# Kernel tuning notes

Measured on AMD Instinct MI355X. Metric: run time of the kernel, lower is better.

## Reference

```python
import jax, jax.numpy as jnp
import numpy as np

B_, T, N, C = 1024, 8, 49, 96
NUM_HEADS = 3
NW = 64  # number of distinct window masks


def setup_inputs() -> dict:
    key = jax.random.key(0)
    ks = jax.random.split(key, 8)
    x = jax.random.normal(ks[0], (B_, T, N, C), dtype=jnp.float32)
    # Swin-style additive mask: mostly 0, some large-negative entries
    mask = jnp.where(jax.random.uniform(ks[1], (NW, N, N)) < 0.9, 0.0, -100.0).astype(jnp.float32)
    s = 0.02
    qkv_w = jax.random.normal(ks[2], (C, 3 * C), dtype=jnp.float32) * s
    qkv_b = jnp.zeros((3 * C,), dtype=jnp.float32)
    proj_sp_w = jax.random.normal(ks[3], (C, C), dtype=jnp.float32) * s
    proj_sp_b = jnp.zeros((C,), dtype=jnp.float32)
    proj_temp_w = jax.random.normal(ks[4], (C, C), dtype=jnp.float32) * s
    proj_temp_b = jnp.zeros((C,), dtype=jnp.float32)
    return {
        "x": x, "mask": mask,
        "qkv_w": qkv_w, "qkv_b": qkv_b,
        "proj_sp_w": proj_sp_w, "proj_sp_b": proj_sp_b,
        "proj_temp_w": proj_temp_w, "proj_temp_b": proj_temp_b,
    }


def _attend(xseq, qkv_w, qkv_b, num_heads, scale, mask=None):
    """xseq: (B, L, C). Returns (B, L, C). mask: (nW, L, L) or None."""
    Bt, L, Cd = xseq.shape
    hd = Cd // num_heads
    qkv = (xseq @ qkv_w + qkv_b).reshape(Bt, L, 3, num_heads, hd)
    q, k, v = qkv[:, :, 0], qkv[:, :, 1], qkv[:, :, 2]  # (B, L, H, hd)
    attn = jnp.einsum("bnhd,bmhd->bhnm", q * scale, k)  # (B, H, L, L)
    if mask is not None:
        nW = mask.shape[0]
        attn = attn.reshape(Bt // nW, nW, num_heads, L, L) + mask[None, :, None]
        attn = attn.reshape(Bt, num_heads, L, L)
    attn = jax.nn.softmax(attn, axis=-1)
    out = jnp.einsum("bhnm,bmhd->bnhd", attn, v).reshape(Bt, L, Cd)
    return out


def reference(x, mask, qkv_w, qkv_b, proj_sp_w, proj_sp_b, proj_temp_w, proj_temp_b):
    Bw, Tt, Nn, Cc = x.shape
    hd = Cc // NUM_HEADS
    scale = hd ** (-0.5)
    # spatial branch: attention over N within each (window, time)
    x_sp = _attend(x.reshape(Bw * Tt, Nn, Cc), qkv_w, qkv_b, NUM_HEADS, scale, mask)
    x_sp = (x_sp @ proj_sp_w + proj_sp_b).reshape(Bw, Tt, Nn, Cc)
    # temporal branch: attention over T for each spatial token
    x_t = x.transpose(0, 2, 1, 3).reshape(Bw * Nn, Tt, Cc)
    x_t = _attend(x_t, qkv_w, qkv_b, NUM_HEADS, scale, None)
    x_t = (x_t @ proj_temp_w + proj_temp_b)
    x_t = x_t.reshape(Bw, Nn, Tt, Cc).transpose(0, 2, 1, 3)
    return (x_t, x_sp)
```

## Files before the change

### kernel.cpp

```cpp
#include <hip/hip_runtime.h>

typedef __bf16 bf16x2 __attribute__((ext_vector_type(2)));
typedef __bf16 bf16x4 __attribute__((ext_vector_type(4)));
typedef __bf16 bf16x8 __attribute__((ext_vector_type(8)));
typedef float f32x4 __attribute__((ext_vector_type(4)));
#define MFMA __builtin_amdgcn_mfma_f32_16x16x32_bf16

#define SCALE 0.17677669529663687f
#define QS2 200
#define VS 72
#define PS 72
#define CS 104

__device__ __forceinline__ bf16x4 cvt4(const float* p) {
  bf16x4 v;
  float4 f = *(const float4*)p;
  v[0] = (__bf16)f.x; v[1] = (__bf16)f.y; v[2] = (__bf16)f.z; v[3] = (__bf16)f.w;
  return v;
}
__device__ __forceinline__ bf16x4 bz4() {
  bf16x4 z;
  for (int i = 0; i < 4; ++i) z[i] = (__bf16)0.f;
  return z;
}

__global__ __launch_bounds__(256) void k_transpose(const float* __restrict__ Wq,
    const float* __restrict__ Wsp, const float* __restrict__ Wtm,
    __bf16* __restrict__ ws) {
  const int which = blockIdx.x, tid = threadIdx.x;
  if (which == 0) {
    for (int idx = tid; idx < 27648; idx += 256) {
      int n = idx / 96, k = idx % 96;
      ws[idx] = (__bf16)Wq[k * 288 + n];
    }
  } else {
    const float* src = (which == 1) ? Wsp : Wtm;
    __bf16* dst = ws + 27648 + (which - 1) * 9216;
    for (int idx = tid; idx < 9216; idx += 256) {
      int n = idx / 96, k = idx % 96;
      dst[idx] = (__bf16)src[k * 96 + n];
    }
  }
}

__global__ __launch_bounds__(512, 4) void k_spatial(const float* __restrict__ x,
    const __bf16* __restrict__ WqT, const float* __restrict__ qkv_b,
    const float* __restrict__ mask, const __bf16* __restrict__ WpT,
    const float* __restrict__ bp, float* __restrict__ out) {
  __shared__ __align__(16) char smem[67072];
  __bf16* qk  = (__bf16*)(smem);
  __bf16* ctx = (__bf16*)(smem);
  __bf16* xt  = (__bf16*)(smem + 25600);
  __bf16* P   = (__bf16*)(smem + 25600);
  __bf16* VT  = (__bf16*)(smem + 53248);

  const int tid = threadIdx.x;
  const int bt = blockIdx.x;
  const long rbase = (long)bt * 49;
  const int wave = tid >> 6, lane = tid & 63, lr = lane & 15, quad = lane >> 4;

  const float* xg = x + rbase * 96;
  for (int v = tid; v < 1536; v += 512) {
    int r = v / 24, c = (v % 24) * 4;
    bf16x4 val = bz4();
    if (r < 49) val = cvt4(&xg[r * 96 + c]);
    *(bf16x4*)&xt[r * CS + c] = val;
  }
  __syncthreads();
  {
    bf16x8 afr[4][3];
    for (int rt = 0; rt < 4; ++rt)
      for (int ks = 0; ks < 3; ++ks)
        afr[rt][ks] = *(const bf16x8*)&xt[(rt * 16 + lr) * CS + ks * 32 + quad * 8];
    for (int ct = wave; ct < 18; ct += 8) {
      const __bf16* wrow = &WqT[(ct * 16 + lr) * 96 + quad * 8];
      bf16x8 b0 = *(const bf16x8*)&wrow[0];
      bf16x8 b1 = *(const bf16x8*)&wrow[32];
      bf16x8 b2 = *(const bf16x8*)&wrow[64];
      int col = ct * 16 + lr;
      float bv = qkv_b[col];
      for (int rt = 0; rt < 4; ++rt) {
        f32x4 acc = {0.f, 0.f, 0.f, 0.f};
        acc = MFMA(afr[rt][0], b0, acc, 0, 0, 0);
        acc = MFMA(afr[rt][1], b1, acc, 0, 0, 0);
        acc = MFMA(afr[rt][2], b2, acc, 0, 0, 0);
        if (ct < 12) {
          for (int i = 0; i < 4; ++i)
            qk[(rt * 16 + quad * 4 + i) * QS2 + col] = (__bf16)(acc[i] + bv);
        } else {
          int d = col - 192;
          __bf16* vp = &VT[d * VS + rt * 16 + quad * 4];
          bf16x2 lo; lo[0] = (__bf16)(acc[0] + bv); lo[1] = (__bf16)(acc[1] + bv);
          bf16x2 hi; hi[0] = (__bf16)(acc[2] + bv); hi[1] = (__bf16)(acc[3] + bv);
          *(bf16x2*)&vp[0] = lo;
          *(bf16x2*)&vp[2] = hi;
        }
      }
    }
  }
  __syncthreads();

  {
    const int rt = wave & 3;
    const int nb = rt * 16 + quad * 4;
    const float* mrow = mask + (long)(bt & 63) * 2401;
    float mv[4][4];
    for (int ct = 0; ct < 4; ++ct) {
      int m = ct * 16 + lr;
      int mm = (m < 49) ? m : 48;
      for (int i = 0; i < 4; ++i) {
        int nn = (nb + i < 49) ? nb + i : 48;
        mv[ct][i] = mrow[nn * 49 + mm];
      }
    }
    for (int task = wave; task < 12; task += 8) {
      int h = task >> 2;
      bf16x8 qf = *(const bf16x8*)&qk[(rt * 16 + lr) * QS2 + h * 32 + quad * 8];
      float sv[4][4];
      for (int ct = 0; ct < 4; ++ct) {
        bf16x8 kf = *(const bf16x8*)&qk[(ct * 16 + lr) * QS2 + 96 + h * 32 + quad * 8];
        f32x4 acc = {0.f, 0.f, 0.f, 0.f};
        acc = MFMA(qf, kf, acc, 0, 0, 0);
        int m = ct * 16 + lr;
        for (int i = 0; i < 4; ++i)
          sv[ct][i] = (m < 49) ? (acc[i] * SCALE + mv[ct][i]) : -1e30f;
      }
      for (int i = 0; i < 4; ++i) {
        float mx = fmaxf(fmaxf(sv[0][i], sv[1][i]), fmaxf(sv[2][i], sv[3][i]));
        mx = fmaxf(mx, __shfl_xor(mx, 1));
        mx = fmaxf(mx, __shfl_xor(mx, 2));
        mx = fmaxf(mx, __shfl_xor(mx, 4));
        mx = fmaxf(mx, __shfl_xor(mx, 8));
        float e0 = __expf(sv[0][i] - mx), e1 = __expf(sv[1][i] - mx);
        float e2 = __expf(sv[2][i] - mx), e3 = __expf(sv[3][i] - mx);
        float sum = e0 + e1 + e2 + e3;
        sum += __shfl_xor(sum, 1);
        sum += __shfl_xor(sum, 2);
        sum += __shfl_xor(sum, 4);
        sum += __shfl_xor(sum, 8);
        float inv = 1.f / sum;
        __bf16* Pr = &P[(h * 64 + nb + i) * PS + lr];
        Pr[0]  = (__bf16)(e0 * inv);
        Pr[16] = (__bf16)(e1 * inv);
        Pr[32] = (__bf16)(e2 * inv);
        Pr[48] = (__bf16)(e3 * inv);
      }
    }
  }
  __syncthreads();

  for (int tile = wave; tile < 24; tile += 8) {
    int h = tile / 8, rt = (tile / 2) & 3, dt = tile & 1;
    f32x4 acc = {0.f, 0.f, 0.f, 0.f};
    for (int ks = 0; ks < 2; ++ks) {
      bf16x8 a  = *(const bf16x8*)&P[(h * 64 + rt * 16 + lr) * PS + ks * 32 + quad * 8];
      bf16x8 bb = *(const bf16x8*)&VT[(h * 32 + dt * 16 + lr) * VS + ks * 32 + quad * 8];
      acc = MFMA(a, bb, acc, 0, 0, 0);
    }
    for (int i = 0; i < 4; ++i)
      ctx[(rt * 16 + quad * 4 + i) * CS + h * 32 + dt * 16 + lr] = (__bf16)acc[i];
  }
  __syncthreads();

  for (int tile = wave; tile < 24; tile += 8) {
    int rt = tile / 6, ct = tile % 6;
    int col = ct * 16 + lr;
    const __bf16* wrow = &WpT[col * 96 + quad * 8];
    f32x4 acc = {0.f, 0.f, 0.f, 0.f};
    for (int ks = 0; ks < 3; ++ks) {
      bf16x8 a  = *(const bf16x8*)&ctx[(rt * 16 + lr) * CS + ks * 32 + quad * 8];
      bf16x8 bb = *(const bf16x8*)&wrow[ks * 32];
      acc = MFMA(a, bb, acc, 0, 0, 0);
    }
    float bv = bp[col];
    for (int i = 0; i < 4; ++i) {
      int r = rt * 16 + quad * 4 + i;
      if (r < 49) out[(rbase + r) * 96 + col] = acc[i] + bv;
    }
  }
}

__global__ __launch_bounds__(512, 4) void k_temporal(const float* __restrict__ x,
    const __bf16* __restrict__ WqT, const float* __restrict__ qkv_b,
    const __bf16* __restrict__ WpT, const float* __restrict__ bp,
    float* __restrict__ out) {
  __shared__ __align__(16) char smem[67072];
  __bf16* qk  = (__bf16*)(smem);
  __bf16* ctx = (__bf16*)(smem);
  __bf16* xt  = (__bf16*)(smem + 25600);
  __bf16* P   = (__bf16*)(smem + 25600);
  __bf16* VT  = (__bf16*)(smem + 53248);

  const int tid = threadIdx.x;
  const int n0 = blockIdx.x * 8;
  const int b = blockIdx.y;
  const int wave = tid >> 6, lane = tid & 63, lr = lane & 15, quad = lane >> 4;

  for (int v = tid; v < 1536; v += 512) {
    int s = v / 24, c = (v % 24) * 4;
    int ni = s >> 3, t = s & 7, n = n0 + ni;
    bf16x4 val = bz4();
    if (n < 49) val = cvt4(&x[((long)(b * 8 + t) * 49 + n) * 96 + c]);
    *(bf16x4*)&xt[s * CS + c] = val;
  }
  __syncthreads();
  {
    bf16x8 afr[4][3];
    for (int rt = 0; rt < 4; ++rt)
      for (int ks = 0; ks < 3; ++ks)
        afr[rt][ks] = *(const bf16x8*)&xt[(rt * 16 + lr) * CS + ks * 32 + quad * 8];
    for (int ct = wave; ct < 18; ct += 8) {
      const __bf16* wrow = &WqT[(ct * 16 + lr) * 96 + quad * 8];
      bf16x8 b0 = *(const bf16x8*)&wrow[0];
      bf16x8 b1 = *(const bf16x8*)&wrow[32];
      bf16x8 b2 = *(const bf16x8*)&wrow[64];
      int col = ct * 16 + lr;
      float bv = qkv_b[col];
      for (int rt = 0; rt < 4; ++rt) {
        f32x4 acc = {0.f, 0.f, 0.f, 0.f};
        acc = MFMA(afr[rt][0], b0, acc, 0, 0, 0);
        acc = MFMA(afr[rt][1], b1, acc, 0, 0, 0);
        acc = MFMA(afr[rt][2], b2, acc, 0, 0, 0);
        if (ct < 12) {
          for (int i = 0; i < 4; ++i)
            qk[(rt * 16 + quad * 4 + i) * QS2 + col] = (__bf16)(acc[i] + bv);
        } else {
          int d = col - 192;
          __bf16* vp = &VT[d * VS + rt * 16 + quad * 4];
          bf16x2 lo; lo[0] = (__bf16)(acc[0] + bv); lo[1] = (__bf16)(acc[1] + bv);
          bf16x2 hi; hi[0] = (__bf16)(acc[2] + bv); hi[1] = (__bf16)(acc[3] + bv);
          *(bf16x2*)&vp[0] = lo;
          *(bf16x2*)&vp[2] = hi;
        }
      }
    }
  }
  __syncthreads();

  {
    const bool useful = (((lane & 15) >> 3) == (lane >> 5));
    for (int task = wave; task < 12; task += 8) {
      int p = task & 3, h = task >> 2;
      bf16x8 qf = *(const bf16x8*)&qk[(p * 16 + lr) * QS2 + h * 32 + quad * 8];
      bf16x8 kf = *(const bf16x8*)&qk[(p * 16 + lr) * QS2 + 96 + h * 32 + quad * 8];
      f32x4 acc = {0.f, 0.f, 0.f, 0.f};
      acc = MFMA(qf, kf, acc, 0, 0, 0);
      for (int rr = 0; rr < 4; ++rr) {
        float s = acc[rr] * SCALE;
        float mx = s;
        mx = fmaxf(mx, __shfl_xor(mx, 1));
        mx = fmaxf(mx, __shfl_xor(mx, 2));
        mx = fmaxf(mx, __shfl_xor(mx, 4));
        float e = __expf(s - mx);
        float sum = e;
        sum += __shfl_xor(sum, 1);
        sum += __shfl_xor(sum, 2);
        sum += __shfl_xor(sum, 4);
        float pv = useful ? (e / sum) : 0.f;
        int row = h * 64 + p * 16 + quad * 4 + rr;
        P[row * PS + p * 16 + (lane & 15)] = (__bf16)pv;
        P[row * PS + (p ^ 1) * 16 + (lane & 15)] = (__bf16)0.f;
      }
    }
  }
  __syncthreads();

  for (int task = wave; task < 24; task += 8) {
    int h = task >> 3, pt = (task >> 1) & 3, dh = task & 1;
    bf16x8 a  = *(const bf16x8*)&P[(h * 64 + pt * 16 + lr) * PS + (pt >> 1) * 32 + quad * 8];
    bf16x8 bb = *(const bf16x8*)&VT[(h * 32 + dh * 16 + lr) * VS + (pt >> 1) * 32 + quad * 8];
    f32x4 acc = {0.f, 0.f, 0.f, 0.f};
    acc = MFMA(a, bb, acc, 0, 0, 0);
    for (int i = 0; i < 4; ++i)
      ctx[(pt * 16 + quad * 4 + i) * CS + h * 32 + dh * 16 + lr] = (__bf16)acc[i];
  }
  __syncthreads();

  for (int tile = wave; tile < 24; tile += 8) {
    int rt = tile / 6, ct = tile % 6;
    int col = ct * 16 + lr;
    const __bf16* wrow = &WpT[col * 96 + quad * 8];
    f32x4 acc = {0.f, 0.f, 0.f, 0.f};
    for (int ks = 0; ks < 3; ++ks) {
      bf16x8 a  = *(const bf16x8*)&ctx[(rt * 16 + lr) * CS + ks * 32 + quad * 8];
      bf16x8 bb = *(const bf16x8*)&wrow[ks * 32];
      acc = MFMA(a, bb, acc, 0, 0, 0);
    }
    float bv = bp[col];
    for (int i = 0; i < 4; ++i) {
      int s = rt * 16 + quad * 4 + i;
      int t = s & 7, n = n0 + (s >> 3);
      if (n < 49) out[((long)(b * 8 + t) * 49 + n) * 96 + col] = acc[i] + bv;
    }
  }
}

extern "C" void kernel_launch(void* const* d_in, const int* in_sizes, int n_in,
                              void* d_out, int out_size, void* d_ws, size_t ws_size,
                              hipStream_t stream) {
  const float* x         = (const float*)d_in[0];
  const float* mask      = (const float*)d_in[1];
  const float* qkv_w     = (const float*)d_in[2];
  const float* qkv_b     = (const float*)d_in[3];
  const float* proj_sp_w = (const float*)d_in[4];
  const float* proj_sp_b = (const float*)d_in[5];
  const float* proj_t_w  = (const float*)d_in[6];
  const float* proj_t_b  = (const float*)d_in[7];
  float* out = (float*)d_out;
  __bf16* wsb = (__bf16*)d_ws;

  const __bf16* WqT  = wsb;
  const __bf16* WspT = wsb + 27648;
  const __bf16* WtmT = wsb + 36864;

  k_transpose<<<dim3(3), dim3(256), 0, stream>>>(qkv_w, proj_sp_w, proj_t_w, wsb);
  k_spatial<<<dim3(8192), dim3(512), 0, stream>>>(x, WqT, qkv_b, mask, WspT,
                                                  proj_sp_b, out + 38535168);
  k_temporal<<<dim3(7, 1024), dim3(512), 0, stream>>>(x, WqT, qkv_b, WtmT,
                                                      proj_t_b, out);
}
```

Before: 665.2 us.

## Fuse spatial and temporal attention into one kernel with 1024-thread blocks

```diff
diff --git a/kernel.cpp b/kernel.cpp
--- a/kernel.cpp
+++ b/kernel.cpp
@@ -11,6 +11,8 @@
 #define VS 72
 #define PS 72
 #define CS 104
+#define NT 1024
+#define WAVES 16
 
 __device__ __forceinline__ bf16x4 cvt4(const float* p) {
   bf16x4 v;
@@ -43,10 +45,12 @@
   }
 }
 
-__global__ __launch_bounds__(512, 4) void k_spatial(const float* __restrict__ x,
+__global__ __launch_bounds__(1024, 8) void k_fused(const float* __restrict__ x,
     const __bf16* __restrict__ WqT, const float* __restrict__ qkv_b,
-    const float* __restrict__ mask, const __bf16* __restrict__ WpT,
-    const float* __restrict__ bp, float* __restrict__ out) {
+    const float* __restrict__ mask,
+    const __bf16* __restrict__ WspT, const float* __restrict__ bsp,
+    const __bf16* __restrict__ WtmT, const float* __restrict__ btm,
+    float* __restrict__ out) {
   __shared__ __align__(16) char smem[67072];
   __bf16* qk  = (__bf16*)(smem);
   __bf16* ctx = (__bf16*)(smem);
@@ -55,16 +59,31 @@
   __bf16* VT  = (__bf16*)(smem + 53248);
 
   const int tid = threadIdx.x;
-  const int bt = blockIdx.x;
-  const long rbase = (long)bt * 49;
   const int wave = tid >> 6, lane = tid & 63, lr = lane & 15, quad = lane >> 4;
-
-  const float* xg = x + rbase * 96;
-  for (int v = tid; v < 1536; v += 512) {
-    int r = v / 24, c = (v % 24) * 4;
-    bf16x4 val = bz4();
-    if (r < 49) val = cvt4(&xg[r * 96 + c]);
-    *(bf16x4*)&xt[r * CS + c] = val;
+  const int bid = blockIdx.x;
+  const bool is_sp = (bid < 8192);
+
+  long rbase = 0; int b = 0, n0 = 0, b0 = 0; bool edge = false;
+  if (is_sp) {
+    rbase = (long)bid * 49;
+  } else if (bid < 14336) {
+    int idx = bid - 8192; b = idx / 6; n0 = (idx % 6) * 8;
+  } else {
+    edge = true; b0 = (bid - 14336) * 8;
+  }
+
+  for (int v = tid; v < 1536; v += NT) {
+    int s = v / 24, c = (v % 24) * 4;
+    bf16x4 val;
+    if (is_sp) {
+      val = bz4();
+      if (s < 49) val = cvt4(&x[(rbase + s) * 96 + c]);
+    } else {
+      long gr = edge ? ((long)((b0 + (s >> 3)) * 8 + (s & 7)) * 49 + 48)
+                     : ((long)(b * 8 + (s & 7)) * 49 + n0 + (s >> 3));
+      val = cvt4(&x[gr * 96 + c]);
+    }
+    *(bf16x4*)&xt[s * CS + c] = val;
   }
   __syncthreads();
   {
@@ -72,18 +91,18 @@
     for (int rt = 0; rt < 4; ++rt)
       for (int ks = 0; ks < 3; ++ks)
         afr[rt][ks] = *(const bf16x8*)&xt[(rt * 16 + lr) * CS + ks * 32 + quad * 8];
-    for (int ct = wave; ct < 18; ct += 8) {
+    for (int ct = wave; ct < 18; ct += WAVES) {
       const __bf16* wrow = &WqT[(ct * 16 + lr) * 96 + quad * 8];
-      bf16x8 b0 = *(const bf16x8*)&wrow[0];
-      bf16x8 b1 = *(const bf16x8*)&wrow[32];
-      bf16x8 b2 = *(const bf16x8*)&wrow[64];
+      bf16x8 b0f = *(const bf16x8*)&wrow[0];
+      bf16x8 b1f = *(const bf16x8*)&wrow[32];
+      bf16x8 b2f = *(const bf16x8*)&wrow[64];
       int col = ct * 16 + lr;
       float bv = qkv_b[col];
       for (int rt = 0; rt < 4; ++rt) {
         f32x4 acc = {0.f, 0.f, 0.f, 0.f};
-        acc = MFMA(afr[rt][0], b0, acc, 0, 0, 0);
-        acc = MFMA(afr[rt][1], b1, acc, 0, 0, 0);
-        acc = MFMA(afr[rt][2], b2, acc, 0, 0, 0);
+        acc = MFMA(afr[rt][0], b0f, acc, 0, 0, 0);
+        acc = MFMA(afr[rt][1], b1f, acc, 0, 0, 0);
+        acc = MFMA(afr[rt][2], b2f, acc, 0, 0, 0);
         if (ct < 12) {
           for (int i = 0; i < 4; ++i)
             qk[(rt * 16 + quad * 4 + i) * QS2 + col] = (__bf16)(acc[i] + bv);
@@ -100,21 +119,20 @@
   }
   __syncthreads();
 
-  {
-    const int rt = wave & 3;
-    const int nb = rt * 16 + quad * 4;
-    const float* mrow = mask + (long)(bt & 63) * 2401;
-    float mv[4][4];
-    for (int ct = 0; ct < 4; ++ct) {
-      int m = ct * 16 + lr;
-      int mm = (m < 49) ? m : 48;
-      for (int i = 0; i < 4; ++i) {
-        int nn = (nb + i < 49) ? nb + i : 48;
-        mv[ct][i] = mrow[nn * 49 + mm];
-      }
-    }
-    for (int task = wave; task < 12; task += 8) {
-      int h = task >> 2;
+  if (is_sp) {
+    if (wave < 12) {
+      const int rt = wave & 3, h = wave >> 2;
+      const int nb = rt * 16 + quad * 4;
+      const float* mrow = mask + (long)(bid & 63) * 2401;
+      float mv[4][4];
+      for (int ct = 0; ct < 4; ++ct) {
+        int m = ct * 16 + lr;
+        int mm = (m < 49) ? m : 48;
+        for (int i = 0; i < 4; ++i) {
+          int nn = (nb + i < 49) ? nb + i : 48;
+          mv[ct][i] = mrow[nn * 49 + mm];
+        }
+      }
       bf16x8 qf = *(const bf16x8*)&qk[(rt * 16 + lr) * QS2 + h * 32 + quad * 8];
       float sv[4][4];
       for (int ct = 0; ct < 4; ++ct) {
@@ -146,101 +164,10 @@
         Pr[48] = (__bf16)(e3 * inv);
       }
     }
-  }
-  __syncthreads();
-
-  for (int tile = wave; tile < 24; tile += 8) {
-    int h = tile / 8, rt = (tile / 2) & 3, dt = tile & 1;
-    f32x4 acc = {0.f, 0.f, 0.f, 0.f};
-    for (int ks = 0; ks < 2; ++ks) {
-      bf16x8 a  = *(const bf16x8*)&P[(h * 64 + rt * 16 + lr) * PS + ks * 32 + quad * 8];
-      bf16x8 bb = *(const bf16x8*)&VT[(h * 32 + dt * 16 + lr) * VS + ks * 32 + quad * 8];
-      acc = MFMA(a, bb, acc, 0, 0, 0);
-    }
-    for (int i = 0; i < 4; ++i)
-      ctx[(rt * 16 + quad * 4 + i) * CS + h * 32 + dt * 16 + lr] = (__bf16)acc[i];
-  }
-  __syncthreads();
-
-  for (int tile = wave; tile < 24; tile += 8) {
-    int rt = tile / 6, ct = tile % 6;
-    int col = ct * 16 + lr;
-    const __bf16* wrow = &WpT[col * 96 + quad * 8];
-    f32x4 acc = {0.f, 0.f, 0.f, 0.f};
-    for (int ks = 0; ks < 3; ++ks) {
-      bf16x8 a  = *(const bf16x8*)&ctx[(rt * 16 + lr) * CS + ks * 32 + quad * 8];
-      bf16x8 bb = *(const bf16x8*)&wrow[ks * 32];
-      acc = MFMA(a, bb, acc, 0, 0, 0);
-    }
-    float bv = bp[col];
-    for (int i = 0; i < 4; ++i) {
-      int r = rt * 16 + quad * 4 + i;
-      if (r < 49) out[(rbase + r) * 96 + col] = acc[i] + bv;
-    }
-  }
-}
-
-__global__ __launch_bounds__(512, 4) void k_temporal(const float* __restrict__ x,
-    const __bf16* __restrict__ WqT, const float* __restrict__ qkv_b,
-    const __bf16* __restrict__ WpT, const float* __restrict__ bp,
-    float* __restrict__ out) {
-  __shared__ __align__(16) char smem[67072];
-  __bf16* qk  = (__bf16*)(smem);
-  __bf16* ctx = (__bf16*)(smem);
-  __bf16* xt  = (__bf16*)(smem + 25600);
-  __bf16* P   = (__bf16*)(smem + 25600);
-  __bf16* VT  = (__bf16*)(smem + 53248);
-
-  const int tid = threadIdx.x;
-  const int n0 = blockIdx.x * 8;
-  const int b = blockIdx.y;
-  const int wave = tid >> 6, lane = tid & 63, lr = lane & 15, quad = lane >> 4;
-
-  for (int v = tid; v < 1536; v += 512) {
-    int s = v / 24, c = (v % 24) * 4;
-    int ni = s >> 3, t = s & 7, n = n0 + ni;
-    bf16x4 val = bz4();
-    if (n < 49) val = cvt4(&x[((long)(b * 8 + t) * 49 + n) * 96 + c]);
-    *(bf16x4*)&xt[s * CS + c] = val;
-  }
-  __syncthreads();
-  {
-    bf16x8 afr[4][3];
-    for (int rt = 0; rt < 4; ++rt)
-      for (int ks = 0; ks < 3; ++ks)
-        afr[rt][ks] = *(const bf16x8*)&xt[(rt * 16 + lr) * CS + ks * 32 + quad * 8];
-    for (int ct = wave; ct < 18; ct += 8) {
-      const __bf16* wrow = &WqT[(ct * 16 + lr) * 96 + quad * 8];
-      bf16x8 b0 = *(const bf16x8*)&wrow[0];
-      bf16x8 b1 = *(const bf16x8*)&wrow[32];
-      bf16x8 b2 = *(const bf16x8*)&wrow[64];
-      int col = ct * 16 + lr;
-      float bv = qkv_b[col];
-      for (int rt = 0; rt < 4; ++rt) {
-        f32x4 acc = {0.f, 0.f, 0.f, 0.f};
-        acc = MFMA(afr[rt][0], b0, acc, 0, 0, 0);
-        acc = MFMA(afr[rt][1], b1, acc, 0, 0, 0);
-        acc = MFMA(afr[rt][2], b2, acc, 0, 0, 0);
-        if (ct < 12) {
-          for (int i = 0; i < 4; ++i)
-            qk[(rt * 16 + quad * 4 + i) * QS2 + col] = (__bf16)(acc[i] + bv);
-        } else {
-          int d = col - 192;
-          __bf16* vp = &VT[d * VS + rt * 16 + quad * 4];
-          bf16x2 lo; lo[0] = (__bf16)(acc[0] + bv); lo[1] = (__bf16)(acc[1] + bv);
-          bf16x2 hi; hi[0] = (__bf16)(acc[2] + bv); hi[1] = (__bf16)(acc[3] + bv);
-          *(bf16x2*)&vp[0] = lo;
-          *(bf16x2*)&vp[2] = hi;
-        }
-      }
-    }
-  }
-  __syncthreads();
-
-  {
-    const bool useful = (((lane & 15) >> 3) == (lane >> 5));
-    for (int task = wave; task < 12; task += 8) {
-      int p = task & 3, h = task >> 2;
+  } else {
+    if (wave < 12) {
+      const bool useful = (((lane & 15) >> 3) == (lane >> 5));
+      int p = wave & 3, h = wave >> 2;
       bf16x8 qf = *(const bf16x8*)&qk[(p * 16 + lr) * QS2 + h * 32 + quad * 8];
       bf16x8 kf = *(const bf16x8*)&qk[(p * 16 + lr) * QS2 + 96 + h * 32 + quad * 8];
       f32x4 acc = {0.f, 0.f, 0.f, 0.f};
@@ -265,32 +192,56 @@
   }
   __syncthreads();
 
-  for (int task = wave; task < 24; task += 8) {
-    int h = task >> 3, pt = (task >> 1) & 3, dh = task & 1;
-    bf16x8 a  = *(const bf16x8*)&P[(h * 64 + pt * 16 + lr) * PS + (pt >> 1) * 32 + quad * 8];
-    bf16x8 bb = *(const bf16x8*)&VT[(h * 32 + dh * 16 + lr) * VS + (pt >> 1) * 32 + quad * 8];
-    f32x4 acc = {0.f, 0.f, 0.f, 0.f};
-    acc = MFMA(a, bb, acc, 0, 0, 0);
-    for (int i = 0; i < 4; ++i)
-      ctx[(pt * 16 + quad * 4 + i) * CS + h * 32 + dh * 16 + lr] = (__bf16)acc[i];
-  }
-  __syncthreads();
-
-  for (int tile = wave; tile < 24; tile += 8) {
-    int rt = tile / 6, ct = tile % 6;
-    int col = ct * 16 + lr;
-    const __bf16* wrow = &WpT[col * 96 + quad * 8];
-    f32x4 acc = {0.f, 0.f, 0.f, 0.f};
-    for (int ks = 0; ks < 3; ++ks) {
-      bf16x8 a  = *(const bf16x8*)&ctx[(rt * 16 + lr) * CS + ks * 32 + quad * 8];
-      bf16x8 bb = *(const bf16x8*)&wrow[ks * 32];
+  if (is_sp) {
+    for (int tile = wave; tile < 24; tile += WAVES) {
+      int h = tile / 8, rt = (tile / 2) & 3, dt = tile & 1;
+      f32x4 acc = {0.f, 0.f, 0.f, 0.f};
+      for (int ks = 0; ks < 2; ++ks) {
+        bf16x8 a  = *(const bf16x8*)&P[(h * 64 + rt * 16 + lr) * PS + ks * 32 + quad * 8];
+        bf16x8 bb = *(const bf16x8*)&VT[(h * 32 + dt * 16 + lr) * VS + ks * 32 + quad * 8];
+        acc = MFMA(a, bb, acc, 0, 0, 0);
+      }
+      for (int i = 0; i < 4; ++i)
+        ctx[(rt * 16 + quad * 4 + i) * CS + h * 32 + dt * 16 + lr] = (__bf16)acc[i];
+    }
+  } else {
+    for (int task = wave; task < 24; task += WAVES) {
+      int h = task >> 3, pt = (task >> 1) & 3, dh = task & 1;
+      bf16x8 a  = *(const bf16x8*)&P[(h * 64 + pt * 16 + lr) * PS + (pt >> 1) * 32 + quad * 8];
+      bf16x8 bb = *(const bf16x8*)&VT[(h * 32 + dh * 16 + lr) * VS + (pt >> 1) * 32 + quad * 8];
+      f32x4 acc = {0.f, 0.f, 0.f, 0.f};
       acc = MFMA(a, bb, acc, 0, 0, 0);
-    }
-    float bv = bp[col];
-    for (int i = 0; i < 4; ++i) {
-      int s = rt * 16 + quad * 4 + i;
-      int t = s & 7, n = n0 + (s >> 3);
-      if (n < 49) out[((long)(b * 8 + t) * 49 + n) * 96 + col] = acc[i] + bv;
+      for (int i = 0; i < 4; ++i)
+        ctx[(pt * 16 + quad * 4 + i) * CS + h * 32 + dh * 16 + lr] = (__bf16)acc[i];
+    }
+  }
+  __syncthreads();
+
+  {
+    const __bf16* Wp = is_sp ? WspT : WtmT;
+    const float* bpv = is_sp ? bsp : btm;
+    float* outp = is_sp ? (out + 38535168) : out;
+    for (int tile = wave; tile < 24; tile += WAVES) {
+      int rt = tile / 6, ct = tile % 6;
+      int col = ct * 16 + lr;
+      const __bf16* wrow = &Wp[col * 96 + quad * 8];
+      f32x4 acc = {0.f, 0.f, 0.f, 0.f};
+      for (int ks = 0; ks < 3; ++ks) {
+        bf16x8 a  = *(const bf16x8*)&ctx[(rt * 16 + lr) * CS + ks * 32 + quad * 8];
+        bf16x8 bb = *(const bf16x8*)&wrow[ks * 32];
+        acc = MFMA(a, bb, acc, 0, 0, 0);
+      }
+      float bv = bpv[col];
+      for (int i = 0; i < 4; ++i) {
+        int s = rt * 16 + quad * 4 + i;
+        if (is_sp) {
+          if (s < 49) outp[(rbase + s) * 96 + col] = acc[i] + bv;
+        } else {
+          long gr = edge ? ((long)((b0 + (s >> 3)) * 8 + (s & 7)) * 49 + 48)
+                         : ((long)(b * 8 + (s & 7)) * 49 + n0 + (s >> 3));
+          outp[gr * 96 + col] = acc[i] + bv;
+        }
+      }
     }
   }
 }
@@ -314,8 +265,7 @@
   const __bf16* WtmT = wsb + 36864;
 
   k_transpose<<<dim3(3), dim3(256), 0, stream>>>(qkv_w, proj_sp_w, proj_t_w, wsb);
-  k_spatial<<<dim3(8192), dim3(512), 0, stream>>>(x, WqT, qkv_b, mask, WspT,
-                                                  proj_sp_b, out + 38535168);
-  k_temporal<<<dim3(7, 1024), dim3(512), 0, stream>>>(x, WqT, qkv_b, WtmT,
-                                                      proj_t_b, out);
-}
+  k_fused<<<dim3(14464), dim3(1024), 0, stream>>>(x, WqT, qkv_b, mask,
+                                                  WspT, proj_sp_b,
+                                                  WtmT, proj_t_b, out);
+}
```

After: 895.0 us. 1.35x slower.
